# Performance work log

Measured on AMD Instinct MI355X. Metric: run time of the kernel, lower is better.

The kernel has to match this reference:

```python
import jax, jax.numpy as jnp
import numpy as np

N_SRC = 200000
N_DST = 50000
N_EDGES = 800000
N_IN = 256
N_OUT = 128


def setup_inputs() -> dict:
    key = jax.random.key(0)
    ks = jax.random.split(key, 10)
    x = jax.random.normal(ks[0], (N_SRC, N_IN), dtype=jnp.float32)
    edge_rows = jax.random.randint(ks[1], (N_EDGES,), 0, N_DST, dtype=jnp.int32)
    edge_cols = jax.random.randint(ks[2], (N_EDGES,), 0, N_SRC, dtype=jnp.int32)
    edge_vals = jax.random.uniform(ks[3], (N_EDGES,), dtype=jnp.float32)
    sampled_nodes = jax.random.randint(ks[4], (N_DST,), 0, N_SRC, dtype=jnp.int32)
    W_w = jax.random.normal(ks[5], (N_IN, N_OUT), dtype=jnp.float32) * 0.05
    b_w = jax.random.normal(ks[6], (N_OUT,), dtype=jnp.float32) * 0.05
    W_b = jax.random.normal(ks[7], (N_IN, N_OUT), dtype=jnp.float32) * 0.05
    b_b = jax.random.normal(ks[8], (N_OUT,), dtype=jnp.float32) * 0.05
    scale = jnp.ones((2 * N_OUT,), dtype=jnp.float32)
    offset = jnp.zeros((2 * N_OUT,), dtype=jnp.float32)
    return {"x": x, "edge_rows": edge_rows, "edge_cols": edge_cols,
            "edge_vals": edge_vals, "sampled_nodes": sampled_nodes,
            "W_w": W_w, "b_w": b_w, "W_b": W_b, "b_b": b_b,
            "scale": scale, "offset": offset}


def reference(x, edge_rows, edge_cols, edge_vals, sampled_nodes,
              W_w, b_w, W_b, b_b, scale, offset):
    # SpMM: feat[r] = sum_e vals[e] * x[cols[e]] for rows[e]==r  -> [N_DST, N_IN]
    msgs = edge_vals[:, None] * x[edge_cols]
    feat = jax.ops.segment_sum(msgs, edge_rows, num_segments=N_DST)
    # dual linear + concat -> [N_DST, 2*N_OUT]
    self_part = x[sampled_nodes] @ W_b + b_b
    neigh_part = feat @ W_w + b_w
    out = jax.nn.elu(jnp.concatenate([self_part, neigh_part], axis=1))
    # row-wise normalize (biased variance), then affine
    mean = out.mean(axis=1, keepdims=True)
    var = out.var(axis=1, keepdims=True) + 1e-9
    return (out - mean) * scale * jax.lax.rsqrt(var) + offset
```

## Files before the change

kernel.cpp:

```cpp
#include <hip/hip_runtime.h>
#include <math.h>

#define N_SRC   200000
#define N_DST   50000
#define N_EDGES 800000
#define N_IN    256
#define N_OUT   128
#define CAP     48

#define WS_CNT   0
#define WS_WTW   3200000
#define WS_WTB   3265536
#define WS_SELF  3331072
#define WS_Y     16131072
#define WS_CSR   67331072

typedef short  bf16x8 __attribute__((ext_vector_type(8)));
typedef unsigned short u16x8 __attribute__((ext_vector_type(8)));
typedef float  f32x4  __attribute__((ext_vector_type(4)));

__device__ inline unsigned short f2bf(float f) {
    unsigned u = __builtin_bit_cast(unsigned, f);
    u += 0x7fffu + ((u >> 16) & 1u);
    return (unsigned short)(u >> 16);
}
__device__ inline float bf2f(unsigned short h) {
    return __builtin_bit_cast(float, (unsigned)h << 16);
}

__global__ __launch_bounds__(256) void k_init(const float* __restrict__ Ww,
                                              const float* __restrict__ Wb,
                                              unsigned short* __restrict__ Wtw,
                                              unsigned short* __restrict__ Wtb,
                                              int* __restrict__ cnt) {
    int tot = blockIdx.x * 256 + threadIdx.x;
    int sel = tot >> 15;
    int idx = tot & 32767;
    int n = idx >> 8, k = idx & 255;
    const float* src = sel ? Wb : Ww;
    unsigned short* dst = sel ? Wtb : Wtw;
    dst[n * 256 + k] = f2bf(src[k * 128 + n]);
    if (tot < N_DST) cnt[tot * 16] = 0;
}

__global__ __launch_bounds__(256) void k_scatter(const int* __restrict__ erows,
                                                 const int* __restrict__ ecols,
                                                 const float* __restrict__ evals,
                                                 int* __restrict__ cnt,
                                                 int2* __restrict__ csr_pad) {
    int i = blockIdx.x * 256 + threadIdx.x;
    int r = erows[i];
    int rank = atomicAdd(&cnt[r * 16], 1);
    if (rank < CAP) {
        int2 cv;
        cv.x = ecols[i];
        cv.y = __builtin_bit_cast(int, evals[i]);
        csr_pad[(long)r * CAP + rank] = cv;
    }
}

#define GBIG  3125
#define GSELF 782
#define EPS 132

#define BSWZ(row, chunk) ((row) * 256 + (((chunk) ^ ((row) & 7)) << 3))

__global__ __launch_bounds__(256, 2) void k_gemm(
        const float* __restrict__ x, const int* __restrict__ sn,
        const unsigned short* __restrict__ Wtw, const unsigned short* __restrict__ Wtb,
        unsigned short* __restrict__ ybuf, unsigned short* __restrict__ selfp) {
    __shared__ __align__(16) unsigned short sm[32768];
    const int tid = threadIdx.x;

    const int gb = blockIdx.x;
    const bool isBig = gb < GBIG;
    const int* rowidx = isBig ? nullptr : sn;
    const unsigned short* Bt = isBig ? Wtw : Wtb;
    unsigned short* Y = isBig ? ybuf : selfp;
    const int M = isBig ? N_SRC : N_DST;
    const int bid = isBig ? gb : gb - GBIG;

    const int lane = tid & 63, wid = tid >> 6;
    const int l15 = lane & 15, quad = lane >> 4;
    const int row0 = bid * 64;

    int srow = row0 + wid * 16 + l15;
    if (srow >= M) srow = M - 1;
    if (rowidx) srow = rowidx[srow];
    const float* ap = x + (long)srow * 256 + quad * 8;

    f32x4 acc[8];
    #pragma unroll
    for (int t = 0; t < 8; t++) acc[t] = (f32x4){0.f, 0.f, 0.f, 0.f};

    u16x8 bst[8];
    #pragma unroll
    for (int j = 0; j < 8; j++)
        bst[j] = ((const u16x8*)Bt)[j * 256 + tid];
    float4 areg[16];
    #pragma unroll
    for (int kt = 0; kt < 8; kt++) {
        areg[2 * kt]     = *(const float4*)(ap + kt * 32);
        areg[2 * kt + 1] = *(const float4*)(ap + kt * 32 + 4);
    }
    __builtin_amdgcn_sched_barrier(0);

    #pragma unroll
    for (int j = 0; j < 8; j++) {
        int slot = j * 256 + tid;
        *(u16x8*)&sm[BSWZ(slot >> 5, slot & 31)] = bst[j];
    }
    #pragma unroll
    for (int j = 0; j < 8; j++)
        bst[j] = ((const u16x8*)Bt)[(j + 8) * 256 + tid];
    __builtin_amdgcn_sched_barrier(0);
    #pragma unroll
    for (int j = 0; j < 8; j++) {
        int slot = (j + 8) * 256 + tid;
        *(u16x8*)&sm[BSWZ(slot >> 5, slot & 31)] = bst[j];
    }
    __syncthreads();

    #pragma unroll
    for (int kt = 0; kt < 8; kt++) {
        float4 a0 = areg[2 * kt], a1 = areg[2 * kt + 1];
        bf16x8 af;
        af[0] = (short)f2bf(a0.x); af[1] = (short)f2bf(a0.y);
        af[2] = (short)f2bf(a0.z); af[3] = (short)f2bf(a0.w);
        af[4] = (short)f2bf(a1.x); af[5] = (short)f2bf(a1.y);
        af[6] = (short)f2bf(a1.z); af[7] = (short)f2bf(a1.w);
        const int chunk = kt * 4 + quad;
        #pragma unroll
        for (int t = 0; t < 8; t++) {
            const int row = t * 16 + l15;
            bf16x8 bfv = *(const bf16x8*)&sm[BSWZ(row, chunk)];
            acc[t] = __builtin_amdgcn_mfma_f32_16x16x32_bf16(af, bfv, acc[t], 0, 0, 0);
        }
    }

    __syncthreads();
    #pragma unroll
    for (int t = 0; t < 8; t++)
        #pragma unroll
        for (int rg = 0; rg < 4; rg++)
            sm[(wid * 16 + quad * 4 + rg) * EPS + t * 16 + l15] = f2bf(acc[t][rg]);
    __syncthreads();
    const int orow = tid >> 2, oc0 = (tid & 3) * 32;
    if (row0 + orow < M) {
        unsigned short* dst = Y + (long)(row0 + orow) * 128 + oc0;
        #pragma unroll
        for (int i = 0; i < 4; i++)
            *(u16x8*)(dst + i * 8) = *(const u16x8*)&sm[orow * EPS + oc0 + i * 8];
    }
}

#define GATHER(j) \
    int   c##j = __shfl(cv.x, e0 + j, 64); \
    float v##j = __builtin_bit_cast(float, __shfl(cv.y, e0 + j, 64)); \
    unsigned p##j = *(const unsigned*)(y + (long)c##j * 128 + (lane << 1));
#define ACCUM(j) \
    a0 = fmaf(v##j, __builtin_bit_cast(float, p##j << 16), a0); \
    a1 = fmaf(v##j, __builtin_bit_cast(float, p##j & 0xffff0000u), a1);

__global__ __launch_bounds__(256) void k_sage(const unsigned short* __restrict__ y,
                                              const unsigned short* __restrict__ selfp,
                                              const int* __restrict__ cnt,
                                              const int2* __restrict__ csr_pad,
                                              const float* __restrict__ bw,
                                              const float* __restrict__ bb,
                                              const float* __restrict__ scale,
                                              const float* __restrict__ offs,
                                              float* __restrict__ out) {
    const int tid = threadIdx.x, lane = tid & 63, wid = tid >> 6;
    const int row = blockIdx.x * 4 + wid;
    const int m = min(cnt[row * 16], CAP);

    int2 cv = (lane < m) ? csr_pad[(long)row * CAP + lane] : make_int2(0, 0);

    unsigned spk = *(const unsigned*)(selfp + (long)row * 128 + lane * 2);
    float s0 = bf2f((unsigned short)(spk & 0xffff)) + bb[lane * 2];
    float s1 = bf2f((unsigned short)(spk >> 16))    + bb[lane * 2 + 1];
    s0 = s0 > 0.f ? s0 : expm1f(s0);
    s1 = s1 > 0.f ? s1 : expm1f(s1);

    float a0 = 0.f, a1 = 0.f;
    const int mm = (m + 7) & ~7;
    for (int e0 = 0; e0 < mm; e0 += 8) {
        GATHER(0) GATHER(1) GATHER(2) GATHER(3)
        GATHER(4) GATHER(5) GATHER(6) GATHER(7)
        ACCUM(0) ACCUM(1) ACCUM(2) ACCUM(3)
        ACCUM(4) ACCUM(5) ACCUM(6) ACCUM(7)
    }
    a0 += bw[lane * 2];
    a1 += bw[lane * 2 + 1];
    a0 = a0 > 0.f ? a0 : expm1f(a0);
    a1 = a1 > 0.f ? a1 : expm1f(a1);

    float s  = s0 + s1 + a0 + a1;
    float s2 = s0 * s0 + s1 * s1 + a0 * a0 + a1 * a1;
    #pragma unroll
    for (int o = 32; o > 0; o >>= 1) {
        s  += __shfl_xor(s,  o, 64);
        s2 += __shfl_xor(s2, o, 64);
    }
    float mean = s * (1.f / 256.f);
    float var  = s2 * (1.f / 256.f) - mean * mean;
    float rstd = rsqrtf(var + 1e-9f);

    float* orow = out + (long)row * 256;
    float2 w0, w1;
    w0.x = (s0 - mean) * rstd * scale[lane * 2]           + offs[lane * 2];
    w0.y = (s1 - mean) * rstd * scale[lane * 2 + 1]       + offs[lane * 2 + 1];
    w1.x = (a0 - mean) * rstd * scale[128 + lane * 2]     + offs[128 + lane * 2];
    w1.y = (a1 - mean) * rstd * scale[128 + lane * 2 + 1] + offs[128 + lane * 2 + 1];
    *(float2*)(orow + lane * 2)       = w0;
    *(float2*)(orow + 128 + lane * 2) = w1;
}

extern "C" void kernel_launch(void* const* d_in, const int* in_sizes, int n_in,
                              void* d_out, int out_size, void* d_ws, size_t ws_size,
                              hipStream_t stream) {
    const float* x     = (const float*)d_in[0];
    const int*   erows = (const int*)  d_in[1];
    const int*   ecols = (const int*)  d_in[2];
    const float* evals = (const float*)d_in[3];
    const int*   sn    = (const int*)  d_in[4];
    const float* Ww    = (const float*)d_in[5];
    const float* bw    = (const float*)d_in[6];
    const float* Wb    = (const float*)d_in[7];
    const float* bb    = (const float*)d_in[8];
    const float* scale = (const float*)d_in[9];
    const float* offs  = (const float*)d_in[10];
    float* out = (float*)d_out;

    char* ws = (char*)d_ws;
    int*   cnt     = (int*)  (ws + WS_CNT);
    unsigned short* Wtw   = (unsigned short*)(ws + WS_WTW);
    unsigned short* Wtb   = (unsigned short*)(ws + WS_WTB);
    unsigned short* selfp = (unsigned short*)(ws + WS_SELF);
    unsigned short* ybuf  = (unsigned short*)(ws + WS_Y);
    int2*  csr_pad = (int2*) (ws + WS_CSR);

    k_init    <<<256, 256, 0, stream>>>(Ww, Wb, Wtw, Wtb, cnt);
    k_scatter <<<N_EDGES / 256, 256, 0, stream>>>(erows, ecols, evals, cnt, csr_pad);
    k_gemm    <<<GBIG + GSELF, 256, 0, stream>>>(x, sn, Wtw, Wtb, ybuf, selfp);
    k_sage    <<<N_DST / 4, 256, 0, stream>>>(ybuf, selfp, cnt, csr_pad,
                                              bw, bb, scale, offs, out);
}
```

Baseline: 424.7 us.

## Fuse edge scatter into persistent double-buffered GEMM with direct permuted stores

Merges the edge-bucketing scatter into the GEMM kernel and turns the GEMM into a persistent grid of 512 blocks that loop over 64-row tiles, prefetching the next tile's A rows into registers while computing the current one. The LDS-staged epilogue is replaced by direct 16-byte stores in a permuted column order, and the aggregation kernel's bias, scale, offset and output indexing are remapped to match that permutation. This removes one launch, the epilogue's LDS round trip and barriers, and the per-tile B reload. In exchange it adds register pressure from double-buffered A tiles and uncoalesced scalar output stores in the final kernel.

```diff
diff --git a/kernel.cpp b/kernel.cpp
--- a/kernel.cpp
+++ b/kernel.cpp
@@ -43,68 +43,100 @@
     if (tot < N_DST) cnt[tot * 16] = 0;
 }
 
-__global__ __launch_bounds__(256) void k_scatter(const int* __restrict__ erows,
-                                                 const int* __restrict__ ecols,
-                                                 const float* __restrict__ evals,
-                                                 int* __restrict__ cnt,
-                                                 int2* __restrict__ csr_pad) {
-    int i = blockIdx.x * 256 + threadIdx.x;
-    int r = erows[i];
-    int rank = atomicAdd(&cnt[r * 16], 1);
-    if (rank < CAP) {
-        int2 cv;
-        cv.x = ecols[i];
-        cv.y = __builtin_bit_cast(int, evals[i]);
-        csr_pad[(long)r * CAP + rank] = cv;
-    }
-}
-
-#define GBIG  3125
-#define GSELF 782
-#define EPS 132
+#define NBBIG 408
+#define NBSLF 104
+#define EPB   1563
 
 #define BSWZ(row, chunk) ((row) * 256 + (((chunk) ^ ((row) & 7)) << 3))
 
-__global__ __launch_bounds__(256, 2) void k_gemm(
-        const float* __restrict__ x, const int* __restrict__ sn,
+#define A_ISSUE(AR, T) do {                                               \
+    int _r = (T) * 64 + wid * 16 + l15;                                   \
+    if (!isBig) { int _c = _r < N_DST ? _r : N_DST - 1; _r = sn[_c]; }    \
+    const float* _ap = x + (long)_r * 256 + quad * 8;                     \
+    _Pragma("unroll")                                                     \
+    for (int _kt = 0; _kt < 8; _kt++) {                                   \
+        AR[2 * _kt]     = *(const float4*)(_ap + _kt * 32);               \
+        AR[2 * _kt + 1] = *(const float4*)(_ap + _kt * 32 + 4);           \
+    }                                                                     \
+} while (0)
+
+#define KLOOP_STORE(AR, T) do {                                           \
+    f32x4 acc[8];                                                         \
+    _Pragma("unroll")                                                     \
+    for (int _t = 0; _t < 8; _t++) acc[_t] = (f32x4){0.f, 0.f, 0.f, 0.f}; \
+    _Pragma("unroll")                                                     \
+    for (int _kt = 0; _kt < 8; _kt++) {                                   \
+        float4 _a0 = AR[2 * _kt], _a1 = AR[2 * _kt + 1];                  \
+        bf16x8 _af;                                                       \
+        _af[0]=(short)f2bf(_a0.x); _af[1]=(short)f2bf(_a0.y);             \
+        _af[2]=(short)f2bf(_a0.z); _af[3]=(short)f2bf(_a0.w);             \
+        _af[4]=(short)f2bf(_a1.x); _af[5]=(short)f2bf(_a1.y);             \
+        _af[6]=(short)f2bf(_a1.z); _af[7]=(short)f2bf(_a1.w);             \
+        const int _ch = _kt * 4 + quad;                                   \
+        _Pragma("unroll")                                                 \
+        for (int _t = 0; _t < 8; _t++) {                                  \
+            bf16x8 _bf = *(const bf16x8*)&sm[BSWZ(_t * 16 + l15, _ch)];   \
+            acc[_t] = __builtin_amdgcn_mfma_f32_16x16x32_bf16(_af, _bf, acc[_t], 0, 0, 0); \
+        }                                                                 \
+    }                                                                     \
+    _Pragma("unroll")                                                     \
+    for (int _rg = 0; _rg < 4; _rg++) {                                   \
+        int _row = (T) * 64 + wid * 16 + quad * 4 + _rg;                  \
+        if (_row < M) {                                                   \
+            u16x8 _w;                                                     \
+            _Pragma("unroll")                                             \
+            for (int _t = 0; _t < 8; _t++) _w[_t] = f2bf(acc[_t][_rg]);   \
+            *(u16x8*)(Y + (long)_row * 128 + l15 * 8) = _w;               \
+        }                                                                 \
+    }                                                                     \
+} while (0)
+
+__global__ __launch_bounds__(256, 2) void k_gemmscat(
+        const float* __restrict__ x,
+        const int* __restrict__ erows, const int* __restrict__ ecols,
+        const float* __restrict__ evals, const int* __restrict__ sn,
         const unsigned short* __restrict__ Wtw, const unsigned short* __restrict__ Wtb,
+        int* __restrict__ cnt, int2* __restrict__ csr_pad,
         unsigned short* __restrict__ ybuf, unsigned short* __restrict__ selfp) {
     __shared__ __align__(16) unsigned short sm[32768];
     const int tid = threadIdx.x;
-
-    const int gb = blockIdx.x;
-    const bool isBig = gb < GBIG;
-    const int* rowidx = isBig ? nullptr : sn;
+    const int bid = blockIdx.x;
+
+    {
+        const int base = bid * EPB;
+        #pragma unroll
+        for (int i = 0; i < 7; i++) {
+            int o = tid + i * 256;
+            int e = base + o;
+            if (o < EPB && e < N_EDGES) {
+                int r = erows[e];
+                int rank = atomicAdd(&cnt[r * 16], 1);
+                if (rank < CAP) {
+                    int2 cv;
+                    cv.x = ecols[e];
+                    cv.y = __builtin_bit_cast(int, evals[e]);
+                    csr_pad[(long)r * CAP + rank] = cv;
+                }
+            }
+        }
+    }
+
+    const bool isBig = bid < NBBIG;
     const unsigned short* Bt = isBig ? Wtw : Wtb;
     unsigned short* Y = isBig ? ybuf : selfp;
-    const int M = isBig ? N_SRC : N_DST;
-    const int bid = isBig ? gb : gb - GBIG;
+    const int M    = isBig ? N_SRC : N_DST;
+    const int t0   = isBig ? bid : bid - NBBIG;
+    const int S    = isBig ? NBBIG : NBSLF;
+    const int tmax = isBig ? 3125 : 782;
 
     const int lane = tid & 63, wid = tid >> 6;
     const int l15 = lane & 15, quad = lane >> 4;
-    const int row0 = bid * 64;
-
-    int srow = row0 + wid * 16 + l15;
-    if (srow >= M) srow = M - 1;
-    if (rowidx) srow = rowidx[srow];
-    const float* ap = x + (long)srow * 256 + quad * 8;
-
-    f32x4 acc[8];
-    #pragma unroll
-    for (int t = 0; t < 8; t++) acc[t] = (f32x4){0.f, 0.f, 0.f, 0.f};
 
     u16x8 bst[8];
     #pragma unroll
     for (int j = 0; j < 8; j++)
         bst[j] = ((const u16x8*)Bt)[j * 256 + tid];
-    float4 areg[16];
-    #pragma unroll
-    for (int kt = 0; kt < 8; kt++) {
-        areg[2 * kt]     = *(const float4*)(ap + kt * 32);
-        areg[2 * kt + 1] = *(const float4*)(ap + kt * 32 + 4);
-    }
     __builtin_amdgcn_sched_barrier(0);
-
     #pragma unroll
     for (int j = 0; j < 8; j++) {
         int slot = j * 256 + tid;
@@ -121,36 +153,21 @@
     }
     __syncthreads();
 
-    #pragma unroll
-    for (int kt = 0; kt < 8; kt++) {
-        float4 a0 = areg[2 * kt], a1 = areg[2 * kt + 1];
-        bf16x8 af;
-        af[0] = (short)f2bf(a0.x); af[1] = (short)f2bf(a0.y);
-        af[2] = (short)f2bf(a0.z); af[3] = (short)f2bf(a0.w);
-        af[4] = (short)f2bf(a1.x); af[5] = (short)f2bf(a1.y);
-        af[6] = (short)f2bf(a1.z); af[7] = (short)f2bf(a1.w);
-        const int chunk = kt * 4 + quad;
-        #pragma unroll
-        for (int t = 0; t < 8; t++) {
-            const int row = t * 16 + l15;
-            bf16x8 bfv = *(const bf16x8*)&sm[BSWZ(row, chunk)];
-            acc[t] = __builtin_amdgcn_mfma_f32_16x16x32_bf16(af, bfv, acc[t], 0, 0, 0);
-        }
-    }
-
-    __syncthreads();
-    #pragma unroll
-    for (int t = 0; t < 8; t++)
-        #pragma unroll
-        for (int rg = 0; rg < 4; rg++)
-            sm[(wid * 16 + quad * 4 + rg) * EPS + t * 16 + l15] = f2bf(acc[t][rg]);
-    __syncthreads();
-    const int orow = tid >> 2, oc0 = (tid & 3) * 32;
-    if (row0 + orow < M) {
-        unsigned short* dst = Y + (long)(row0 + orow) * 128 + oc0;
-        #pragma unroll
-        for (int i = 0; i < 4; i++)
-            *(u16x8*)(dst + i * 8) = *(const u16x8*)&sm[orow * EPS + oc0 + i * 8];
+    float4 pa[16], qa[16];
+    int t = t0;
+    A_ISSUE(pa, t);
+    while (true) {
+        int t1 = t + S; int t1e = t1 < tmax ? t1 : t;
+        A_ISSUE(qa, t1e);
+        __builtin_amdgcn_sched_barrier(0);
+        KLOOP_STORE(pa, t);
+        if (t1 >= tmax) break;
+        int t2 = t1 + S; int t2e = t2 < tmax ? t2 : t1;
+        A_ISSUE(pa, t2e);
+        __builtin_amdgcn_sched_barrier(0);
+        KLOOP_STORE(qa, t1);
+        if (t2 >= tmax) break;
+        t = t2;
     }
 }
 
@@ -175,11 +192,15 @@
     const int row = blockIdx.x * 4 + wid;
     const int m = min(cnt[row * 16], CAP);
 
+    const int c0p = 2 * lane, c1p = 2 * lane + 1;
+    const int j0 = ((c0p & 7) << 4) | (c0p >> 3);
+    const int j1 = ((c1p & 7) << 4) | (c1p >> 3);
+
     int2 cv = (lane < m) ? csr_pad[(long)row * CAP + lane] : make_int2(0, 0);
 
     unsigned spk = *(const unsigned*)(selfp + (long)row * 128 + lane * 2);
-    float s0 = bf2f((unsigned short)(spk & 0xffff)) + bb[lane * 2];
-    float s1 = bf2f((unsigned short)(spk >> 16))    + bb[lane * 2 + 1];
+    float s0 = bf2f((unsigned short)(spk & 0xffff)) + bb[j0];
+    float s1 = bf2f((unsigned short)(spk >> 16))    + bb[j1];
     s0 = s0 > 0.f ? s0 : expm1f(s0);
     s1 = s1 > 0.f ? s1 : expm1f(s1);
 
@@ -191,8 +212,8 @@
         ACCUM(0) ACCUM(1) ACCUM(2) ACCUM(3)
         ACCUM(4) ACCUM(5) ACCUM(6) ACCUM(7)
     }
-    a0 += bw[lane * 2];
-    a1 += bw[lane * 2 + 1];
+    a0 += bw[j0];
+    a1 += bw[j1];
     a0 = a0 > 0.f ? a0 : expm1f(a0);
     a1 = a1 > 0.f ? a1 : expm1f(a1);
 
@@ -208,13 +229,10 @@
     float rstd = rsqrtf(var + 1e-9f);
 
     float* orow = out + (long)row * 256;
-    float2 w0, w1;
-    w0.x = (s0 - mean) * rstd * scale[lane * 2]           + offs[lane * 2];
-    w0.y = (s1 - mean) * rstd * scale[lane * 2 + 1]       + offs[lane * 2 + 1];
-    w1.x = (a0 - mean) * rstd * scale[128 + lane * 2]     + offs[128 + lane * 2];
-    w1.y = (a1 - mean) * rstd * scale[128 + lane * 2 + 1] + offs[128 + lane * 2 + 1];
-    *(float2*)(orow + lane * 2)       = w0;
-    *(float2*)(orow + 128 + lane * 2) = w1;
+    orow[j0]       = (s0 - mean) * rstd * scale[j0]       + offs[j0];
+    orow[j1]       = (s1 - mean) * rstd * scale[j1]       + offs[j1];
+    orow[128 + j0] = (a0 - mean) * rstd * scale[128 + j0] + offs[128 + j0];
+    orow[128 + j1] = (a1 - mean) * rstd * scale[128 + j1] + offs[128 + j1];
 }
 
 extern "C" void kernel_launch(void* const* d_in, const int* in_sizes, int n_in,
@@ -241,9 +259,9 @@
     unsigned short* ybuf  = (unsigned short*)(ws + WS_Y);
     int2*  csr_pad = (int2*) (ws + WS_CSR);
 
-    k_init    <<<256, 256, 0, stream>>>(Ww, Wb, Wtw, Wtb, cnt);
-    k_scatter <<<N_EDGES / 256, 256, 0, stream>>>(erows, ecols, evals, cnt, csr_pad);
-    k_gemm    <<<GBIG + GSELF, 256, 0, stream>>>(x, sn, Wtw, Wtb, ybuf, selfp);
-    k_sage    <<<N_DST / 4, 256, 0, stream>>>(ybuf, selfp, cnt, csr_pad,
-                                              bw, bb, scale, offs, out);
-}
+    k_init     <<<256, 256, 0, stream>>>(Ww, Wb, Wtw, Wtb, cnt);
+    k_gemmscat <<<NBBIG + NBSLF, 256, 0, stream>>>(x, erows, ecols, evals, sn,
+                                                   Wtw, Wtb, cnt, csr_pad, ybuf, selfp);
+    k_sage     <<<N_DST / 4, 256, 0, stream>>>(ybuf, selfp, cnt, csr_pad,
+                                               bw, bb, scale, offs, out);
+}
```

After: 416.4 us. About the same (-2.0%).

## Double-buffer GEMM via direct global-to-LDS loads and store permuted output columns

Applied to the files above, without the earlier changes.

The projection GEMM now streams A and B tiles straight into shared memory with global_load_lds, double-buffered across eight K steps. This replaces register staging of the full weight matrix and whole A rows, halves LDS use and raises occupancy from two to four blocks. The epilogue writes bf16 rows directly in a permuted column order rather than transposing through LDS, and the sage kernel undoes that permutation when applying bias, scale and offset, at the cost of scattered scalar output stores. The gather loop is also unrolled to sixteen edges per iteration. Risks are the per-step barrier, correctness of the swizzle and permutation mapping, and less coalesced output writes.

```diff
diff --git a/kernel.cpp b/kernel.cpp
--- a/kernel.cpp
+++ b/kernel.cpp
@@ -18,6 +18,9 @@
 typedef short  bf16x8 __attribute__((ext_vector_type(8)));
 typedef unsigned short u16x8 __attribute__((ext_vector_type(8)));
 typedef float  f32x4  __attribute__((ext_vector_type(4)));
+
+typedef const __attribute__((address_space(1))) void gv_t;
+typedef __attribute__((address_space(3))) void lv_t;
 
 __device__ inline unsigned short f2bf(float f) {
     unsigned u = __builtin_bit_cast(unsigned, f);
@@ -61,96 +64,99 @@
 
 #define GBIG  3125
 #define GSELF 782
-#define EPS 132
-
-#define BSWZ(row, chunk) ((row) * 256 + (((chunk) ^ ((row) & 7)) << 3))
-
-__global__ __launch_bounds__(256, 2) void k_gemm(
+
+__global__ __launch_bounds__(256, 4) void k_gemm(
         const float* __restrict__ x, const int* __restrict__ sn,
         const unsigned short* __restrict__ Wtw, const unsigned short* __restrict__ Wtb,
         unsigned short* __restrict__ ybuf, unsigned short* __restrict__ selfp) {
-    __shared__ __align__(16) unsigned short sm[32768];
+    __shared__ __align__(16) unsigned short sm[16384];
+    unsigned short* Ab[2] = { sm,        sm + 4096 };
+    unsigned short* Bb[2] = { sm + 8192, sm + 12288 };
+
     const int tid = threadIdx.x;
-
-    const int gb = blockIdx.x;
-    const bool isBig = gb < GBIG;
-    const int* rowidx = isBig ? nullptr : sn;
+    const int bid = blockIdx.x;
+    const bool isBig = bid < GBIG;
     const unsigned short* Bt = isBig ? Wtw : Wtb;
     unsigned short* Y = isBig ? ybuf : selfp;
-    const int M = isBig ? N_SRC : N_DST;
-    const int bid = isBig ? gb : gb - GBIG;
+    const int M    = isBig ? N_SRC : N_DST;
+    const int tile = isBig ? bid : bid - GBIG;
 
     const int lane = tid & 63, wid = tid >> 6;
     const int l15 = lane & 15, quad = lane >> 4;
-    const int row0 = bid * 64;
-
-    int srow = row0 + wid * 16 + l15;
-    if (srow >= M) srow = M - 1;
-    if (rowidx) srow = rowidx[srow];
-    const float* ap = x + (long)srow * 256 + quad * 8;
+
+    const char* xb = (const char*)x;
+    long abase[2];
+    #pragma unroll
+    for (int q = 0; q < 2; q++) {
+        int rl = (wid * 2 + q) * 8 + (lane >> 3);
+        int row = tile * 64 + rl;
+        if (row >= M) row = M - 1;
+        if (!isBig) row = sn[row];
+        abase[q] = (long)row * 1024 + (long)(((lane & 7) ^ ((lane >> 3) & 7)) << 4);
+    }
+    const char* btb = (const char*)Bt;
+    long bbase[2];
+    #pragma unroll
+    for (int q = 0; q < 2; q++) {
+        int row = (wid * 2 + q) * 16 + (lane >> 2);
+        bbase[q] = (long)row * 512 + (long)(((lane & 3) ^ ((lane >> 3) & 3)) << 4);
+    }
 
     f32x4 acc[8];
     #pragma unroll
     for (int t = 0; t < 8; t++) acc[t] = (f32x4){0.f, 0.f, 0.f, 0.f};
 
-    u16x8 bst[8];
-    #pragma unroll
-    for (int j = 0; j < 8; j++)
-        bst[j] = ((const u16x8*)Bt)[j * 256 + tid];
-    float4 areg[16];
+    #pragma unroll
+    for (int q = 0; q < 2; q++) {
+        __builtin_amdgcn_global_load_lds((gv_t*)(xb + abase[q]),
+            (lv_t*)(Ab[0] + (wid * 2 + q) * 512), 16, 0, 0);
+        __builtin_amdgcn_global_load_lds((gv_t*)(btb + bbase[q]),
+            (lv_t*)(Bb[0] + (wid * 2 + q) * 512), 16, 0, 0);
+    }
+    __syncthreads();
+
+    const int arow = (wid * 16 + l15) * 64;
+    const int aswz = l15 & 7;
+    const int bswz = quad ^ ((l15 >> 1) & 3);
+    int cur = 0;
     #pragma unroll
     for (int kt = 0; kt < 8; kt++) {
-        areg[2 * kt]     = *(const float4*)(ap + kt * 32);
-        areg[2 * kt + 1] = *(const float4*)(ap + kt * 32 + 4);
-    }
-    __builtin_amdgcn_sched_barrier(0);
-
-    #pragma unroll
-    for (int j = 0; j < 8; j++) {
-        int slot = j * 256 + tid;
-        *(u16x8*)&sm[BSWZ(slot >> 5, slot & 31)] = bst[j];
-    }
-    #pragma unroll
-    for (int j = 0; j < 8; j++)
-        bst[j] = ((const u16x8*)Bt)[(j + 8) * 256 + tid];
-    __builtin_amdgcn_sched_barrier(0);
-    #pragma unroll
-    for (int j = 0; j < 8; j++) {
-        int slot = (j + 8) * 256 + tid;
-        *(u16x8*)&sm[BSWZ(slot >> 5, slot & 31)] = bst[j];
-    }
-    __syncthreads();
-
-    #pragma unroll
-    for (int kt = 0; kt < 8; kt++) {
-        float4 a0 = areg[2 * kt], a1 = areg[2 * kt + 1];
+        if (kt < 7) {
+            #pragma unroll
+            for (int q = 0; q < 2; q++) {
+                __builtin_amdgcn_global_load_lds((gv_t*)(xb + abase[q] + (kt + 1) * 128),
+                    (lv_t*)(Ab[cur ^ 1] + (wid * 2 + q) * 512), 16, 0, 0);
+                __builtin_amdgcn_global_load_lds((gv_t*)(btb + bbase[q] + (kt + 1) * 64),
+                    (lv_t*)(Bb[cur ^ 1] + (wid * 2 + q) * 512), 16, 0, 0);
+            }
+        }
+        const unsigned short* A = Ab[cur];
+        const unsigned short* B = Bb[cur];
+        float4 a0 = *(const float4*)&A[arow + (((quad * 2)     ^ aswz) << 3)];
+        float4 a1 = *(const float4*)&A[arow + (((quad * 2 + 1) ^ aswz) << 3)];
         bf16x8 af;
         af[0] = (short)f2bf(a0.x); af[1] = (short)f2bf(a0.y);
         af[2] = (short)f2bf(a0.z); af[3] = (short)f2bf(a0.w);
         af[4] = (short)f2bf(a1.x); af[5] = (short)f2bf(a1.y);
         af[6] = (short)f2bf(a1.z); af[7] = (short)f2bf(a1.w);
-        const int chunk = kt * 4 + quad;
         #pragma unroll
         for (int t = 0; t < 8; t++) {
-            const int row = t * 16 + l15;
-            bf16x8 bfv = *(const bf16x8*)&sm[BSWZ(row, chunk)];
-            acc[t] = __builtin_amdgcn_mfma_f32_16x16x32_bf16(af, bfv, acc[t], 0, 0, 0);
+            bf16x8 bv = *(const bf16x8*)&B[(t * 16 + l15) * 32 + (bswz << 3)];
+            acc[t] = __builtin_amdgcn_mfma_f32_16x16x32_bf16(af, bv, acc[t], 0, 0, 0);
         }
-    }
-
-    __syncthreads();
-    #pragma unroll
-    for (int t = 0; t < 8; t++)
-        #pragma unroll
-        for (int rg = 0; rg < 4; rg++)
-            sm[(wid * 16 + quad * 4 + rg) * EPS + t * 16 + l15] = f2bf(acc[t][rg]);
-    __syncthreads();
-    const int orow = tid >> 2, oc0 = (tid & 3) * 32;
-    if (row0 + orow < M) {
-        unsigned short* dst = Y + (long)(row0 + orow) * 128 + oc0;
-        #pragma unroll
-        for (int i = 0; i < 4; i++)
-            *(u16x8*)(dst + i * 8) = *(const u16x8*)&sm[orow * EPS + oc0 + i * 8];
+        __syncthreads();
+        cur ^= 1;
+    }
+
+    #pragma unroll
+    for (int rg = 0; rg < 4; rg++) {
+        int row = tile * 64 + wid * 16 + quad * 4 + rg;
+        if (row < M) {
+            u16x8 w;
+            #pragma unroll
+            for (int t = 0; t < 8; t++) w[t] = f2bf(acc[t][rg]);
+            *(u16x8*)(Y + (long)row * 128 + l15 * 8) = w;
+        }
     }
 }
 
@@ -175,24 +181,32 @@
     const int row = blockIdx.x * 4 + wid;
     const int m = min(cnt[row * 16], CAP);
 
+    const int c0p = 2 * lane, c1p = 2 * lane + 1;
+    const int j0 = ((c0p & 7) << 4) | (c0p >> 3);
+    const int j1 = ((c1p & 7) << 4) | (c1p >> 3);
+
     int2 cv = (lane < m) ? csr_pad[(long)row * CAP + lane] : make_int2(0, 0);
 
     unsigned spk = *(const unsigned*)(selfp + (long)row * 128 + lane * 2);
-    float s0 = bf2f((unsigned short)(spk & 0xffff)) + bb[lane * 2];
-    float s1 = bf2f((unsigned short)(spk >> 16))    + bb[lane * 2 + 1];
+    float s0 = bf2f((unsigned short)(spk & 0xffff)) + bb[j0];
+    float s1 = bf2f((unsigned short)(spk >> 16))    + bb[j1];
     s0 = s0 > 0.f ? s0 : expm1f(s0);
     s1 = s1 > 0.f ? s1 : expm1f(s1);
 
     float a0 = 0.f, a1 = 0.f;
-    const int mm = (m + 7) & ~7;
-    for (int e0 = 0; e0 < mm; e0 += 8) {
-        GATHER(0) GATHER(1) GATHER(2) GATHER(3)
-        GATHER(4) GATHER(5) GATHER(6) GATHER(7)
-        ACCUM(0) ACCUM(1) ACCUM(2) ACCUM(3)
-        ACCUM(4) ACCUM(5) ACCUM(6) ACCUM(7)
-    }
-    a0 += bw[lane * 2];
-    a1 += bw[lane * 2 + 1];
+    const int mm = (m + 15) & ~15;
+    for (int e0 = 0; e0 < mm; e0 += 16) {
+        GATHER(0)  GATHER(1)  GATHER(2)  GATHER(3)
+        GATHER(4)  GATHER(5)  GATHER(6)  GATHER(7)
+        GATHER(8)  GATHER(9)  GATHER(10) GATHER(11)
+        GATHER(12) GATHER(13) GATHER(14) GATHER(15)
+        ACCUM(0)  ACCUM(1)  ACCUM(2)  ACCUM(3)
+        ACCUM(4)  ACCUM(5)  ACCUM(6)  ACCUM(7)
+        ACCUM(8)  ACCUM(9)  ACCUM(10) ACCUM(11)
+        ACCUM(12) ACCUM(13) ACCUM(14) ACCUM(15)
+    }
+    a0 += bw[j0];
+    a1 += bw[j1];
     a0 = a0 > 0.f ? a0 : expm1f(a0);
     a1 = a1 > 0.f ? a1 : expm1f(a1);
 
@@ -208,13 +222,10 @@
     float rstd = rsqrtf(var + 1e-9f);
 
     float* orow = out + (long)row * 256;
-    float2 w0, w1;
-    w0.x = (s0 - mean) * rstd * scale[lane * 2]           + offs[lane * 2];
-    w0.y = (s1 - mean) * rstd * scale[lane * 2 + 1]       + offs[lane * 2 + 1];
-    w1.x = (a0 - mean) * rstd * scale[128 + lane * 2]     + offs[128 + lane * 2];
-    w1.y = (a1 - mean) * rstd * scale[128 + lane * 2 + 1] + offs[128 + lane * 2 + 1];
-    *(float2*)(orow + lane * 2)       = w0;
-    *(float2*)(orow + 128 + lane * 2) = w1;
+    orow[j0]       = (s0 - mean) * rstd * scale[j0]       + offs[j0];
+    orow[j1]       = (s1 - mean) * rstd * scale[j1]       + offs[j1];
+    orow[128 + j0] = (a0 - mean) * rstd * scale[128 + j0] + offs[128 + j0];
+    orow[128 + j1] = (a1 - mean) * rstd * scale[128 + j1] + offs[128 + j1];
 }
 
 extern "C" void kernel_launch(void* const* d_in, const int* in_sizes, int n_in,
```

New measurement: 434.6 us. 1.02x slower.
